# Kernel tuning notes

Hardware: AMD Instinct MI355X
Metric: run time of the kernel (lower is better)

Reference implementation:

```python
import jax, jax.numpy as jnp
import numpy as np

B, L, H, NH, NB = 16, 200, 128, 2, 2
ITEMS, SPAN = 50000, 256
NEG = -2.0**32 + 1.0  # mask value used by the torch module


def _ln(x, g, b, eps=1e-8):
    m = jnp.mean(x, axis=-1, keepdims=True)
    v = jnp.mean((x - m) ** 2, axis=-1, keepdims=True)
    return (x - m) / jnp.sqrt(v + eps) * g + b


def setup_inputs() -> dict:
    key = jax.random.key(0)
    ks = jax.random.split(key, 20)
    p = lambda k, s: (jax.random.normal(k, s, jnp.float32) * 0.02)
    item_emb = p(ks[0], (ITEMS + 1, H)).at[0].set(0.0)  # padding_idx=0
    return {
        "user_ids": jax.random.randint(ks[1], (B,), 0, 10000),
        "log_seqs": jax.random.randint(ks[2], (B, L), 0, ITEMS),
        "time_matrices": jax.random.randint(ks[3], (B, L, L), 0, SPAN),
        "pos_seqs": jax.random.randint(ks[4], (B, L), 0, ITEMS),
        "neg_seqs": jax.random.randint(ks[5], (B, L), 0, ITEMS),
        "item_emb": item_emb,
        "pos_K_emb": p(ks[6], (L, H)),
        "pos_V_emb": p(ks[7], (L, H)),
        "time_K_emb": p(ks[8], (SPAN + 1, H)),
        "time_V_emb": p(ks[9], (SPAN + 1, H)),
        "Wq": p(ks[10], (NB, H, H)), "bq": jnp.zeros((NB, H)),
        "Wk": p(ks[11], (NB, H, H)), "bk": jnp.zeros((NB, H)),
        "Wv": p(ks[12], (NB, H, H)), "bv": jnp.zeros((NB, H)),
        "ln1_g": jnp.ones((NB, H)), "ln1_b": jnp.zeros((NB, H)),
        "W1": p(ks[13], (NB, H, H)), "b1": jnp.zeros((NB, H)),
        "W2": p(ks[14], (NB, H, H)), "b2": jnp.zeros((NB, H)),
        "ln2_g": jnp.ones((NB, H)), "ln2_b": jnp.zeros((NB, H)),
        "lnf_g": jnp.ones((H,)), "lnf_b": jnp.zeros((H,)),
    }


def reference(user_ids, log_seqs, time_matrices, pos_seqs, neg_seqs,
              item_emb, pos_K_emb, pos_V_emb, time_K_emb, time_V_emb,
              Wq, bq, Wk, bk, Wv, bv, ln1_g, ln1_b,
              W1, b1, W2, b2, ln2_g, ln2_b, lnf_g, lnf_b):
    d = H // NH
    pad = (log_seqs == 0)                    # (B,L) timeline mask
    keep = (~pad)[..., None].astype(jnp.float32)

    seqs = item_emb[log_seqs] * jnp.sqrt(jnp.float32(H))
    seqs = seqs * keep
    posK = pos_K_emb.reshape(L, NH, d)       # same for every batch element
    posV = pos_V_emb.reshape(L, NH, d)
    tmK = time_K_emb[time_matrices].reshape(B, L, L, NH, d)  # (B,L,L,h,d)
    tmV = time_V_emb[time_matrices].reshape(B, L, L, NH, d)
    causal = ~jnp.tril(jnp.ones((L, L), dtype=bool))          # True = masked
    mask = pad[:, None, :, None] | causal[None, None, :, :]   # (B,1,L,L) row-mask | causal

    for i in range(NB):
        Q = (seqs @ Wq[i].T + bq[i]).reshape(B, L, NH, d)
        K = (seqs @ Wk[i].T + bk[i]).reshape(B, L, NH, d)
        V = (seqs @ Wv[i].T + bv[i]).reshape(B, L, NH, d)
        aw = jnp.einsum('bqhd,bkhd->bhqk', Q, K)
        aw = aw + jnp.einsum('bqhd,khd->bhqk', Q, posK)
        aw = aw + jnp.einsum('bqkhd,bqhd->bhqk', tmK, Q)
        aw = aw / jnp.sqrt(jnp.float32(d))
        aw = jnp.where(mask, NEG, aw)
        A = jax.nn.softmax(aw, axis=-1)                        # (B,h,L,L)
        out = jnp.einsum('bhqk,bkhd->bqhd', A, V)
        out = out + jnp.einsum('bhqk,khd->bqhd', A, posV)
        out = out + jnp.einsum('bhqk,bqkhd->bqhd', A, tmV)
        out = out.reshape(B, L, H)
        seqs = _ln(seqs + out, ln1_g[i], ln1_b[i])
        ffn = jax.nn.relu(seqs @ W1[i].T + b1[i]) @ W2[i].T + b2[i]
        seqs = _ln(seqs + ffn, ln2_g[i], ln2_b[i])
        seqs = seqs * keep

    log_feats = _ln(seqs, lnf_g, lnf_b)
    pos_logits = jnp.sum(log_feats * item_emb[pos_seqs], axis=-1)  # (B,L)
    neg_logits = jnp.sum(log_feats * item_emb[neg_seqs], axis=-1)
    return jnp.stack([pos_logits, neg_logits])  # (2,B,L)
```

## Files before the change

kernel.cpp:

```cpp
#include <hip/hip_runtime.h>
#include <hip/hip_bf16.h>
#include <math.h>

#define BB 16
#define LL 200
#define HH 128
#define DD 64
#define QT2 8
#define NQT2 25
#define NEGF -4294967295.0f
#define SQRTH 11.313708498984761f

__global__ __launch_bounds__(512) void k_qkv(float* __restrict__ seqs,
    const int* __restrict__ log_seqs, const float* __restrict__ item_emb, int do_embed,
    const float* __restrict__ Wq, const float* __restrict__ bq,
    const float* __restrict__ Wk, const float* __restrict__ bk,
    const float* __restrict__ Wv, const float* __restrict__ bv,
    const float* __restrict__ posK, const float* __restrict__ posV,
    float* __restrict__ Q, float* __restrict__ Kp, float* __restrict__ Vp) {
    __shared__ float s_lds[16][HH];
    int r0g = blockIdx.x * 16;
    int t = threadIdx.x;
    if (do_embed) {
        int r = t >> 5, d4 = t & 31;
        int id = log_seqs[r0g + r];
        float4 v = make_float4(0.f, 0.f, 0.f, 0.f);
        if (id != 0) {
            v = ((const float4*)(item_emb + id * HH))[d4];
            v.x *= SQRTH; v.y *= SQRTH; v.z *= SQRTH; v.w *= SQRTH;
        }
        *(float4*)&s_lds[r][d4 * 4] = v;
        ((float4*)(seqs + r0g * HH))[t] = v;
    } else {
        ((float4*)s_lds)[t] = ((const float4*)(seqs + r0g * HH))[t];
    }
    __syncthreads();
    int c = t & 127, rg = t >> 7;
    float aq[4] = {0.f, 0.f, 0.f, 0.f};
    float ak[4] = {0.f, 0.f, 0.f, 0.f};
    float av[4] = {0.f, 0.f, 0.f, 0.f};
    const float4* wq4 = (const float4*)(Wq + c * HH);
    const float4* wk4 = (const float4*)(Wk + c * HH);
    const float4* wv4 = (const float4*)(Wv + c * HH);
#pragma unroll 4
    for (int k4 = 0; k4 < HH / 4; ++k4) {
        float4 wq = wq4[k4], wk = wk4[k4], wv = wv4[k4];
#pragma unroll
        for (int r = 0; r < 4; ++r) {
            float4 s = *(const float4*)&s_lds[rg * 4 + r][k4 * 4];
            aq[r] += s.x * wq.x + s.y * wq.y + s.z * wq.z + s.w * wq.w;
            ak[r] += s.x * wk.x + s.y * wk.y + s.z * wk.z + s.w * wk.w;
            av[r] += s.x * wv.x + s.y * wv.y + s.z * wv.z + s.w * wv.w;
        }
    }
#pragma unroll
    for (int r = 0; r < 4; ++r) {
        int row = r0g + rg * 4 + r;
        int l = row % LL;
        Q[row * HH + c]  = aq[r] + bq[c];
        Kp[row * HH + c] = ak[r] + bk[c] + posK[l * HH + c];
        Vp[row * HH + c] = av[r] + bv[c] + posV[l * HH + c];
    }
}

__global__ __launch_bounds__(256) void k_proj(const float* __restrict__ Q,
    const float* __restrict__ timeK, float* __restrict__ projK) {
    int bh = blockIdx.x / 13, qt = blockIdx.x % 13;
    int b = bh >> 1, h = bh & 1;
    int qlo = qt * 16;
    __shared__ float Qs[16][68];
    __shared__ float TK[32][68];
    int t = threadIdx.x;
    {
        int r = t >> 4, d4 = t & 15;
        int q = qlo + r;
        float4 v = make_float4(0.f, 0.f, 0.f, 0.f);
        if (q < LL) v = ((const float4*)(Q + (b * LL + q) * HH + h * DD))[d4];
        *(float4*)&Qs[r][d4 * 4] = v;
    }
    int tq = t >> 4, ttl = t & 15;
    int q = qlo + tq;
    for (int c = 0; c < 9; ++c) {
        int base = c * 32;
        __syncthreads();
        for (int x = t; x < 512; x += 256) {
            int i = x >> 4, d4 = x & 15;
            int tt = base + i;
            if (tt < 257)
                *(float4*)&TK[i][d4 * 4] =
                    ((const float4*)(timeK + tt * HH + h * DD))[d4];
        }
        __syncthreads();
#pragma unroll
        for (int j = 0; j < 2; ++j) {
            int ti = ttl + 16 * j;
            int tt = base + ti;
            if (tt < 257 && q < LL) {
                float acc = 0.f;
#pragma unroll
                for (int d4 = 0; d4 < 16; ++d4) {
                    float4 qv = *(const float4*)&Qs[tq][d4 * 4];
                    float4 kv = *(const float4*)&TK[ti][d4 * 4];
                    acc += qv.x * kv.x + qv.y * kv.y + qv.z * kv.z + qv.w * kv.w;
                }
                projK[(bh * LL + q) * 257 + tt] = acc;
            }
        }
    }
}

__global__ __launch_bounds__(256) void k_attn(
    const float* __restrict__ Q, const float* __restrict__ Kp, const float* __restrict__ Vp,
    const float* __restrict__ projK, const float* __restrict__ timeV,
    const int* __restrict__ tm, const int* __restrict__ log_seqs,
    float* __restrict__ attnout) {
    int bh = blockIdx.x / NQT2, qt = blockIdx.x % NQT2;
    int b = bh >> 1, h = bh & 1;
    int qlo = qt * QT2;
    __shared__ float K_s[32][68];
    __shared__ float smemW[457 * 12];
    __shared__ float proj_T[257][9];
    __shared__ unsigned long long pm64[4];
    __shared__ int s_allmask;
#define WT(i, j) smemW[(i) * 12 + (j)]
    int t = threadIdx.x;
    int tq = t >> 5, lane = t & 31, g = tq;
    int q = qlo + tq;
    int qhi = qlo + QT2 - 1;

    {
        bool keep = (t < LL) && (log_seqs[b * LL + t] != 0);
        unsigned long long ball = __ballot(keep);
        if ((t & 63) == 0) pm64[t >> 6] = ball;
    }
    if (t == 0) s_allmask = 0;
    for (int x = t; x < 200 * 12; x += 256) smemW[x] = NEGF;
    for (int x = 200 * 12 + t; x < 457 * 12; x += 256) smemW[x] = 0.f;
    {
        const float* pbase = projK + (bh * LL + qlo) * 257;
        for (int x = t; x < 8 * 257; x += 256) {
            int qq = x / 257, tt = x - qq * 257;
            proj_T[tt][qq] = pbase[x];
        }
    }
    float4 qreg[16];
    {
        const float4* qp = (const float4*)(Q + (b * LL + q) * HH + h * DD);
#pragma unroll
        for (int d4 = 0; d4 < 16; ++d4) qreg[d4] = qp[d4];
    }
    const int* tmrow = tm + (b * LL + q) * LL;
    __syncthreads();

    int nkc = (qhi >> 5) + 1;
    for (int kc = 0; kc < nkc; ++kc) {
        int kbase = kc * 32;
        for (int x = t; x < 512; x += 256) {
            int i = x >> 4, d4 = x & 15;
            int k = kbase + i;
            if (k < LL)
                *(float4*)&K_s[i][d4 * 4] =
                    ((const float4*)(Kp + (b * LL + k) * HH + h * DD))[d4];
        }
        __syncthreads();
        int k = kbase + lane;
        if (k <= q && ((pm64[k >> 6] >> (k & 63)) & 1ull)) {
            float acc = 0.f;
#pragma unroll
            for (int d4 = 0; d4 < 16; ++d4) {
                float4 kv = *(const float4*)&K_s[lane][d4 * 4];
                acc += qreg[d4].x * kv.x + qreg[d4].y * kv.y +
                       qreg[d4].z * kv.z + qreg[d4].w * kv.w;
            }
            WT(k, tq) = (acc + proj_T[tmrow[k]][tq]) * 0.125f;
        }
        __syncthreads();
    }

    float mx = -INFINITY;
    for (int k = lane; k < LL; k += 32) mx = fmaxf(mx, WT(k, tq));
    mx = fmaxf(mx, __shfl_xor(mx, 1, 64));
    mx = fmaxf(mx, __shfl_xor(mx, 2, 64));
    mx = fmaxf(mx, __shfl_xor(mx, 4, 64));
    mx = fmaxf(mx, __shfl_xor(mx, 8, 64));
    mx = fmaxf(mx, __shfl_xor(mx, 16, 64));
    bool allmask = (mx == NEGF);
    float sum = 0.f;
    for (int k = lane; k < LL; k += 32) {
        float e = __expf(WT(k, tq) - mx);
        WT(k, tq) = e;
        sum += e;
    }
    sum += __shfl_xor(sum, 1, 64);
    sum += __shfl_xor(sum, 2, 64);
    sum += __shfl_xor(sum, 4, 64);
    sum += __shfl_xor(sum, 8, 64);
    sum += __shfl_xor(sum, 16, 64);
    float inv = 1.0f / sum;
    int klim = allmask ? LL : (q + 1);
    if (allmask && lane == 0) s_allmask = 1;
    for (int k = lane; k < LL; k += 32) {
        float p = WT(k, tq) * inv;
        WT(k, tq) = p;
        if (k < klim) atomicAdd(&WT(200 + tmrow[k], tq), p);
    }
    __syncthreads();

    int kmax = s_allmask ? LL : (qhi + 1);
    float a00=0.f,a01=0.f,a10=0.f,a11=0.f,a20=0.f,a21=0.f,a30=0.f,a31=0.f;
    float a40=0.f,a41=0.f,a50=0.f,a51=0.f,a60=0.f,a61=0.f,a70=0.f,a71=0.f;
#define PV_STEP(WROW, SRCPTR)                                            \
    {                                                                    \
        const float* wr = &WROW;                                         \
        float4 w0 = *(const float4*)wr;                                  \
        float4 w1 = *(const float4*)(wr + 4);                            \
        float2 vv = *(const float2*)(SRCPTR);                            \
        a00 += w0.x * vv.x; a01 += w0.x * vv.y;                          \
        a10 += w0.y * vv.x; a11 += w0.y * vv.y;                          \
        a20 += w0.z * vv.x; a21 += w0.z * vv.y;                          \
        a30 += w0.w * vv.x; a31 += w0.w * vv.y;                          \
        a40 += w1.x * vv.x; a41 += w1.x * vv.y;                          \
        a50 += w1.y * vv.x; a51 += w1.y * vv.y;                          \
        a60 += w1.z * vv.x; a61 += w1.z * vv.y;                          \
        a70 += w1.w * vv.x; a71 += w1.w * vv.y;                          \
    }
    for (int i = g; i < kmax; i += 8)
        PV_STEP(WT(i, 0), Vp + (b * LL + i) * HH + h * DD + lane * 2);
    for (int i = g; i < 257; i += 8)
        PV_STEP(WT(200 + i, 0), timeV + i * HH + h * DD + lane * 2);
#undef PV_STEP
    __syncthreads();
    float* part = smemW;
    part[g * 512 + 0 * 64 + lane * 2] = a00; part[g * 512 + 0 * 64 + lane * 2 + 1] = a01;
    part[g * 512 + 1 * 64 + lane * 2] = a10; part[g * 512 + 1 * 64 + lane * 2 + 1] = a11;
    part[g * 512 + 2 * 64 + lane * 2] = a20; part[g * 512 + 2 * 64 + lane * 2 + 1] = a21;
    part[g * 512 + 3 * 64 + lane * 2] = a30; part[g * 512 + 3 * 64 + lane * 2 + 1] = a31;
    part[g * 512 + 4 * 64 + lane * 2] = a40; part[g * 512 + 4 * 64 + lane * 2 + 1] = a41;
    part[g * 512 + 5 * 64 + lane * 2] = a50; part[g * 512 + 5 * 64 + lane * 2 + 1] = a51;
    part[g * 512 + 6 * 64 + lane * 2] = a60; part[g * 512 + 6 * 64 + lane * 2 + 1] = a61;
    part[g * 512 + 7 * 64 + lane * 2] = a70; part[g * 512 + 7 * 64 + lane * 2 + 1] = a71;
    __syncthreads();
    {
        float ox = 0.f, oy = 0.f;
#pragma unroll
        for (int gg = 0; gg < 8; ++gg) {
            ox += part[gg * 512 + tq * 64 + lane * 2];
            oy += part[gg * 512 + tq * 64 + lane * 2 + 1];
        }
        *(float2*)(attnout + (b * LL + q) * HH + h * DD + lane * 2) =
            make_float2(ox, oy);
    }
#undef WT
}

__global__ __launch_bounds__(256) void k_ffn_full(
    float* __restrict__ seqs, const float* __restrict__ AO,
    const float* __restrict__ g1, const float* __restrict__ be1,
    const float* __restrict__ W1, const float* __restrict__ b1,
    const float* __restrict__ W2, const float* __restrict__ b2,
    const float* __restrict__ g2, const float* __restrict__ be2,
    const int* __restrict__ log_seqs) {
    __shared__ float s_lds[8][HH];
    __shared__ float h_lds[8][HH];
    int r0g = blockIdx.x * 8;
    int t = threadIdx.x;
    {
        float4 a = ((const float4*)(seqs + r0g * HH))[t];
        float4 o = ((const float4*)(AO + r0g * HH))[t];
        a.x += o.x; a.y += o.y; a.z += o.z; a.w += o.w;
        ((float4*)s_lds)[t] = a;
    }
    __syncthreads();
    int w = t >> 6, lane = t & 63;
    int lrow = w * 2 + (lane >> 5), cl = lane & 31;
    {
        float sm = 0.f;
#pragma unroll
        for (int j = 0; j < 4; ++j) sm += s_lds[lrow][cl + 32 * j];
        sm += __shfl_xor(sm, 1, 64);
        sm += __shfl_xor(sm, 2, 64);
        sm += __shfl_xor(sm, 4, 64);
        sm += __shfl_xor(sm, 8, 64);
        sm += __shfl_xor(sm, 16, 64);
        float mean = sm * (1.0f / HH);
        float vr = 0.f;
#pragma unroll
        for (int j = 0; j < 4; ++j) {
            float d = s_lds[lrow][cl + 32 * j] - mean;
            vr += d * d;
        }
        vr += __shfl_xor(vr, 1, 64);
        vr += __shfl_xor(vr, 2, 64);
        vr += __shfl_xor(vr, 4, 64);
        vr += __shfl_xor(vr, 8, 64);
        vr += __shfl_xor(vr, 16, 64);
        float rstd = rsqrtf(vr * (1.0f / HH) + 1e-8f);
#pragma unroll
        for (int j = 0; j < 4; ++j) {
            int c = cl + 32 * j;
            s_lds[lrow][c] = (s_lds[lrow][c] - mean) * rstd * g1[c] + be1[c];
        }
    }
    __syncthreads();
    int c = t & 127, rg = t >> 7;
    float acc[4] = {0.f, 0.f, 0.f, 0.f};
    const float4* w14 = (const float4*)(W1 + c * HH);
#pragma unroll 4
    for (int k4 = 0; k4 < HH / 4; ++k4) {
        float4 ww = w14[k4];
#pragma unroll
        for (int r = 0; r < 4; ++r) {
            float4 s = *(const float4*)&s_lds[rg * 4 + r][k4 * 4];
            acc[r] += s.x * ww.x + s.y * ww.y + s.z * ww.z + s.w * ww.w;
        }
    }
#pragma unroll
    for (int r = 0; r < 4; ++r) h_lds[rg * 4 + r][c] = fmaxf(acc[r] + b1[c], 0.f);
    __syncthreads();
#pragma unroll
    for (int r = 0; r < 4; ++r) acc[r] = 0.f;
    const float4* w24 = (const float4*)(W2 + c * HH);
#pragma unroll 4
    for (int k4 = 0; k4 < HH / 4; ++k4) {
        float4 ww = w24[k4];
#pragma unroll
        for (int r = 0; r < 4; ++r) {
            float4 s = *(const float4*)&h_lds[rg * 4 + r][k4 * 4];
            acc[r] += s.x * ww.x + s.y * ww.y + s.z * ww.z + s.w * ww.w;
        }
    }
    __syncthreads();
#pragma unroll
    for (int r = 0; r < 4; ++r)
        h_lds[rg * 4 + r][c] = s_lds[rg * 4 + r][c] + acc[r] + b2[c];
    __syncthreads();
    {
        float sm = 0.f;
#pragma unroll
        for (int j = 0; j < 4; ++j) sm += h_lds[lrow][cl + 32 * j];
        sm += __shfl_xor(sm, 1, 64);
        sm += __shfl_xor(sm, 2, 64);
        sm += __shfl_xor(sm, 4, 64);
        sm += __shfl_xor(sm, 8, 64);
        sm += __shfl_xor(sm, 16, 64);
        float mean = sm * (1.0f / HH);
        float vr = 0.f;
#pragma unroll
        for (int j = 0; j < 4; ++j) {
            float d = h_lds[lrow][cl + 32 * j] - mean;
            vr += d * d;
        }
        vr += __shfl_xor(vr, 1, 64);
        vr += __shfl_xor(vr, 2, 64);
        vr += __shfl_xor(vr, 4, 64);
        vr += __shfl_xor(vr, 8, 64);
        vr += __shfl_xor(vr, 16, 64);
        float rstd = rsqrtf(vr * (1.0f / HH) + 1e-8f);
        float keep = (log_seqs[r0g + lrow] != 0) ? 1.0f : 0.0f;
#pragma unroll
        for (int j = 0; j < 4; ++j) {
            int cc = cl + 32 * j;
            float y = (h_lds[lrow][cc] - mean) * rstd * g2[cc] + be2[cc];
            seqs[(r0g + lrow) * HH + cc] = y * keep;
        }
    }
}

__global__ void k_final(const float* __restrict__ seqs,
                        const float* __restrict__ lnf_g, const float* __restrict__ lnf_b,
                        const float* __restrict__ item_emb,
                        const int* __restrict__ pos_seqs, const int* __restrict__ neg_seqs,
                        float* __restrict__ out) {
    __shared__ float red[2];
    int row = blockIdx.x;
    int t = threadIdx.x;
    float x = seqs[row * HH + t];
    float m = x;
    m += __shfl_xor(m, 1, 64); m += __shfl_xor(m, 2, 64); m += __shfl_xor(m, 4, 64);
    m += __shfl_xor(m, 8, 64); m += __shfl_xor(m, 16, 64); m += __shfl_xor(m, 32, 64);
    if ((t & 63) == 0) red[t >> 6] = m;
    __syncthreads();
    m = (red[0] + red[1]) * (1.0f / HH);
    float d = x - m;
    __syncthreads();
    float v2 = d * d;
    v2 += __shfl_xor(v2, 1, 64); v2 += __shfl_xor(v2, 2, 64); v2 += __shfl_xor(v2, 4, 64);
    v2 += __shfl_xor(v2, 8, 64); v2 += __shfl_xor(v2, 16, 64); v2 += __shfl_xor(v2, 32, 64);
    if ((t & 63) == 0) red[t >> 6] = v2;
    __syncthreads();
    float var = (red[0] + red[1]) * (1.0f / HH);
    float lf = d * rsqrtf(var + 1e-8f) * lnf_g[t] + lnf_b[t];
    int pid = pos_seqs[row];
    int nid = neg_seqs[row];
    float pp = lf * item_emb[pid * HH + t];
    float nn = lf * item_emb[nid * HH + t];
    __syncthreads();
    float ps = pp;
    ps += __shfl_xor(ps, 1, 64); ps += __shfl_xor(ps, 2, 64); ps += __shfl_xor(ps, 4, 64);
    ps += __shfl_xor(ps, 8, 64); ps += __shfl_xor(ps, 16, 64); ps += __shfl_xor(ps, 32, 64);
    if ((t & 63) == 0) red[t >> 6] = ps;
    __syncthreads();
    float ptot = red[0] + red[1];
    __syncthreads();
    float ns = nn;
    ns += __shfl_xor(ns, 1, 64); ns += __shfl_xor(ns, 2, 64); ns += __shfl_xor(ns, 4, 64);
    ns += __shfl_xor(ns, 8, 64); ns += __shfl_xor(ns, 16, 64); ns += __shfl_xor(ns, 32, 64);
    if ((t & 63) == 0) red[t >> 6] = ns;
    __syncthreads();
    float ntot = red[0] + red[1];
    if (t == 0) {
        out[row] = ptot;
        out[BB * LL + row] = ntot;
    }
}

extern "C" void kernel_launch(void* const* d_in, const int* in_sizes, int n_in,
                              void* d_out, int out_size, void* d_ws, size_t ws_size,
                              hipStream_t stream) {
    const int* log_seqs = (const int*)d_in[1];
    const int* tm       = (const int*)d_in[2];
    const int* pos_seqs = (const int*)d_in[3];
    const int* neg_seqs = (const int*)d_in[4];
    const float* item_emb = (const float*)d_in[5];
    const float* posK   = (const float*)d_in[6];
    const float* posV   = (const float*)d_in[7];
    const float* timeK  = (const float*)d_in[8];
    const float* timeV  = (const float*)d_in[9];
    const float* Wq = (const float*)d_in[10];
    const float* bq = (const float*)d_in[11];
    const float* Wk = (const float*)d_in[12];
    const float* bk = (const float*)d_in[13];
    const float* Wv = (const float*)d_in[14];
    const float* bv = (const float*)d_in[15];
    const float* ln1_g = (const float*)d_in[16];
    const float* ln1_b = (const float*)d_in[17];
    const float* W1 = (const float*)d_in[18];
    const float* b1 = (const float*)d_in[19];
    const float* W2 = (const float*)d_in[20];
    const float* b2 = (const float*)d_in[21];
    const float* ln2_g = (const float*)d_in[22];
    const float* ln2_b = (const float*)d_in[23];
    const float* lnf_g = (const float*)d_in[24];
    const float* lnf_b = (const float*)d_in[25];

    float* ws    = (float*)d_ws;
    float* seqs  = ws;
    float* Qb    = seqs + 409600;
    float* Kpb   = Qb + 409600;
    float* Vpb   = Kpb + 409600;
    float* AO    = Vpb + 409600;
    float* projK = AO + 409600;

    for (int i = 0; i < 2; ++i) {
        k_qkv<<<BB * LL / 16, 512, 0, stream>>>(seqs, log_seqs, item_emb, (i == 0) ? 1 : 0,
            Wq + i * HH * HH, bq + i * HH,
            Wk + i * HH * HH, bk + i * HH,
            Wv + i * HH * HH, bv + i * HH,
            posK, posV, Qb, Kpb, Vpb);
        k_proj<<<32 * 13, 256, 0, stream>>>(Qb, timeK, projK);
        k_attn<<<32 * NQT2, 256, 0, stream>>>(Qb, Kpb, Vpb, projK, timeV,
                                              tm, log_seqs, AO);
        k_ffn_full<<<BB * LL / 8, 256, 0, stream>>>(seqs, AO,
            ln1_g + i * HH, ln1_b + i * HH,
            W1 + i * HH * HH, b1 + i * HH,
            W2 + i * HH * HH, b2 + i * HH,
            ln2_g + i * HH, ln2_b + i * HH, log_seqs);
    }
    k_final<<<BB * LL, HH, 0, stream>>>(seqs, lnf_g, lnf_b, item_emb,
                                        pos_seqs, neg_seqs, (float*)d_out);
}
```

Baseline: 198.4 us.

## Fuse time-key projection into QKV kernel and final LN/logits into FFN kernel

```diff
diff --git a/kernel.cpp b/kernel.cpp
--- a/kernel.cpp
+++ b/kernel.cpp
@@ -11,14 +11,17 @@
 #define NEGF -4294967295.0f
 #define SQRTH 11.313708498984761f
 
-__global__ __launch_bounds__(512) void k_qkv(float* __restrict__ seqs,
+__global__ __launch_bounds__(512) void k_qkv_proj(float* __restrict__ seqs,
     const int* __restrict__ log_seqs, const float* __restrict__ item_emb, int do_embed,
     const float* __restrict__ Wq, const float* __restrict__ bq,
     const float* __restrict__ Wk, const float* __restrict__ bk,
     const float* __restrict__ Wv, const float* __restrict__ bv,
     const float* __restrict__ posK, const float* __restrict__ posV,
-    float* __restrict__ Q, float* __restrict__ Kp, float* __restrict__ Vp) {
+    const float* __restrict__ timeK,
+    float* __restrict__ Q, float* __restrict__ Kp, float* __restrict__ Vp,
+    float* __restrict__ projK) {
     __shared__ float s_lds[16][HH];
+    __shared__ float TK[32][132];
     int r0g = blockIdx.x * 16;
     int t = threadIdx.x;
     if (do_embed) {
@@ -53,57 +56,42 @@
             av[r] += s.x * wv.x + s.y * wv.y + s.z * wv.z + s.w * wv.w;
         }
     }
+    __syncthreads();
 #pragma unroll
     for (int r = 0; r < 4; ++r) {
         int row = r0g + rg * 4 + r;
         int l = row % LL;
-        Q[row * HH + c]  = aq[r] + bq[c];
+        float qv = aq[r] + bq[c];
+        Q[row * HH + c]  = qv;
+        s_lds[rg * 4 + r][c] = qv;
         Kp[row * HH + c] = ak[r] + bk[c] + posK[l * HH + c];
         Vp[row * HH + c] = av[r] + bv[c] + posV[l * HH + c];
     }
-}
-
-__global__ __launch_bounds__(256) void k_proj(const float* __restrict__ Q,
-    const float* __restrict__ timeK, float* __restrict__ projK) {
-    int bh = blockIdx.x / 13, qt = blockIdx.x % 13;
-    int b = bh >> 1, h = bh & 1;
-    int qlo = qt * 16;
-    __shared__ float Qs[16][68];
-    __shared__ float TK[32][68];
-    int t = threadIdx.x;
-    {
-        int r = t >> 4, d4 = t & 15;
-        int q = qlo + r;
-        float4 v = make_float4(0.f, 0.f, 0.f, 0.f);
-        if (q < LL) v = ((const float4*)(Q + (b * LL + q) * HH + h * DD))[d4];
-        *(float4*)&Qs[r][d4 * 4] = v;
-    }
-    int tq = t >> 4, ttl = t & 15;
-    int q = qlo + tq;
-    for (int c = 0; c < 9; ++c) {
-        int base = c * 32;
+    int tq = t >> 5, ttl = t & 31;
+    int row = r0g + tq;
+    int brow = row / LL, lrow = row - brow * LL;
+    for (int ch = 0; ch < 9; ++ch) {
+        int base = ch * 32;
         __syncthreads();
-        for (int x = t; x < 512; x += 256) {
-            int i = x >> 4, d4 = x & 15;
+        for (int x = t; x < 32 * 32; x += 512) {
+            int i = x >> 5, d4 = x & 31;
             int tt = base + i;
             if (tt < 257)
-                *(float4*)&TK[i][d4 * 4] =
-                    ((const float4*)(timeK + tt * HH + h * DD))[d4];
+                *(float4*)&TK[i][d4 * 4] = ((const float4*)(timeK + tt * HH))[d4];
         }
         __syncthreads();
-#pragma unroll
-        for (int j = 0; j < 2; ++j) {
-            int ti = ttl + 16 * j;
-            int tt = base + ti;
-            if (tt < 257 && q < LL) {
+        int tt = base + ttl;
+        if (tt < 257) {
+#pragma unroll
+            for (int h = 0; h < 2; ++h) {
                 float acc = 0.f;
 #pragma unroll
                 for (int d4 = 0; d4 < 16; ++d4) {
-                    float4 qv = *(const float4*)&Qs[tq][d4 * 4];
-                    float4 kv = *(const float4*)&TK[ti][d4 * 4];
+                    float4 qv = *(const float4*)&s_lds[tq][h * DD + d4 * 4];
+                    float4 kv = *(const float4*)&TK[ttl][h * DD + d4 * 4];
                     acc += qv.x * kv.x + qv.y * kv.y + qv.z * kv.z + qv.w * kv.w;
                 }
-                projK[(bh * LL + q) * 257 + tt] = acc;
+                projK[((brow * 2 + h) * LL + lrow) * 257 + tt] = acc;
             }
         }
     }
@@ -253,16 +241,20 @@
 #undef WT
 }
 
-__global__ __launch_bounds__(256) void k_ffn_full(
+__global__ __launch_bounds__(512) void k_ffn_full(
     float* __restrict__ seqs, const float* __restrict__ AO,
     const float* __restrict__ g1, const float* __restrict__ be1,
     const float* __restrict__ W1, const float* __restrict__ b1,
     const float* __restrict__ W2, const float* __restrict__ b2,
     const float* __restrict__ g2, const float* __restrict__ be2,
-    const int* __restrict__ log_seqs) {
-    __shared__ float s_lds[8][HH];
-    __shared__ float h_lds[8][HH];
-    int r0g = blockIdx.x * 8;
+    const int* __restrict__ log_seqs, int do_final,
+    const float* __restrict__ lnf_g, const float* __restrict__ lnf_b,
+    const float* __restrict__ item_emb,
+    const int* __restrict__ pos_seqs, const int* __restrict__ neg_seqs,
+    float* __restrict__ out) {
+    __shared__ float s_lds[16][HH];
+    __shared__ float h_lds[16][HH];
+    int r0g = blockIdx.x * 16;
     int t = threadIdx.x;
     {
         float4 a = ((const float4*)(seqs + r0g * HH))[t];
@@ -356,61 +348,63 @@
         vr += __shfl_xor(vr, 8, 64);
         vr += __shfl_xor(vr, 16, 64);
         float rstd = rsqrtf(vr * (1.0f / HH) + 1e-8f);
-        float keep = (log_seqs[r0g + lrow] != 0) ? 1.0f : 0.0f;
+        int row = r0g + lrow;
+        float keep = (log_seqs[row] != 0) ? 1.0f : 0.0f;
+        float y2[4];
 #pragma unroll
         for (int j = 0; j < 4; ++j) {
             int cc = cl + 32 * j;
-            float y = (h_lds[lrow][cc] - mean) * rstd * g2[cc] + be2[cc];
-            seqs[(r0g + lrow) * HH + cc] = y * keep;
-        }
-    }
-}
-
-__global__ void k_final(const float* __restrict__ seqs,
-                        const float* __restrict__ lnf_g, const float* __restrict__ lnf_b,
-                        const float* __restrict__ item_emb,
-                        const int* __restrict__ pos_seqs, const int* __restrict__ neg_seqs,
-                        float* __restrict__ out) {
-    __shared__ float red[2];
-    int row = blockIdx.x;
-    int t = threadIdx.x;
-    float x = seqs[row * HH + t];
-    float m = x;
-    m += __shfl_xor(m, 1, 64); m += __shfl_xor(m, 2, 64); m += __shfl_xor(m, 4, 64);
-    m += __shfl_xor(m, 8, 64); m += __shfl_xor(m, 16, 64); m += __shfl_xor(m, 32, 64);
-    if ((t & 63) == 0) red[t >> 6] = m;
-    __syncthreads();
-    m = (red[0] + red[1]) * (1.0f / HH);
-    float d = x - m;
-    __syncthreads();
-    float v2 = d * d;
-    v2 += __shfl_xor(v2, 1, 64); v2 += __shfl_xor(v2, 2, 64); v2 += __shfl_xor(v2, 4, 64);
-    v2 += __shfl_xor(v2, 8, 64); v2 += __shfl_xor(v2, 16, 64); v2 += __shfl_xor(v2, 32, 64);
-    if ((t & 63) == 0) red[t >> 6] = v2;
-    __syncthreads();
-    float var = (red[0] + red[1]) * (1.0f / HH);
-    float lf = d * rsqrtf(var + 1e-8f) * lnf_g[t] + lnf_b[t];
-    int pid = pos_seqs[row];
-    int nid = neg_seqs[row];
-    float pp = lf * item_emb[pid * HH + t];
-    float nn = lf * item_emb[nid * HH + t];
-    __syncthreads();
-    float ps = pp;
-    ps += __shfl_xor(ps, 1, 64); ps += __shfl_xor(ps, 2, 64); ps += __shfl_xor(ps, 4, 64);
-    ps += __shfl_xor(ps, 8, 64); ps += __shfl_xor(ps, 16, 64); ps += __shfl_xor(ps, 32, 64);
-    if ((t & 63) == 0) red[t >> 6] = ps;
-    __syncthreads();
-    float ptot = red[0] + red[1];
-    __syncthreads();
-    float ns = nn;
-    ns += __shfl_xor(ns, 1, 64); ns += __shfl_xor(ns, 2, 64); ns += __shfl_xor(ns, 4, 64);
-    ns += __shfl_xor(ns, 8, 64); ns += __shfl_xor(ns, 16, 64); ns += __shfl_xor(ns, 32, 64);
-    if ((t & 63) == 0) red[t >> 6] = ns;
-    __syncthreads();
-    float ntot = red[0] + red[1];
-    if (t == 0) {
-        out[row] = ptot;
-        out[BB * LL + row] = ntot;
+            y2[j] = ((h_lds[lrow][cc] - mean) * rstd * g2[cc] + be2[cc]) * keep;
+        }
+        if (!do_final) {
+#pragma unroll
+            for (int j = 0; j < 4; ++j)
+                seqs[row * HH + cl + 32 * j] = y2[j];
+        } else {
+            float sm2 = y2[0] + y2[1] + y2[2] + y2[3];
+            sm2 += __shfl_xor(sm2, 1, 64);
+            sm2 += __shfl_xor(sm2, 2, 64);
+            sm2 += __shfl_xor(sm2, 4, 64);
+            sm2 += __shfl_xor(sm2, 8, 64);
+            sm2 += __shfl_xor(sm2, 16, 64);
+            float mean2 = sm2 * (1.0f / HH);
+            float vr2 = 0.f;
+#pragma unroll
+            for (int j = 0; j < 4; ++j) {
+                float d = y2[j] - mean2;
+                vr2 += d * d;
+            }
+            vr2 += __shfl_xor(vr2, 1, 64);
+            vr2 += __shfl_xor(vr2, 2, 64);
+            vr2 += __shfl_xor(vr2, 4, 64);
+            vr2 += __shfl_xor(vr2, 8, 64);
+            vr2 += __shfl_xor(vr2, 16, 64);
+            float rstd2 = rsqrtf(vr2 * (1.0f / HH) + 1e-8f);
+            int pid = pos_seqs[row];
+            int nid = neg_seqs[row];
+            float pp = 0.f, nn = 0.f;
+#pragma unroll
+            for (int j = 0; j < 4; ++j) {
+                int cc = cl + 32 * j;
+                float lf = (y2[j] - mean2) * rstd2 * lnf_g[cc] + lnf_b[cc];
+                pp += lf * item_emb[pid * HH + cc];
+                nn += lf * item_emb[nid * HH + cc];
+            }
+            pp += __shfl_xor(pp, 1, 64);
+            pp += __shfl_xor(pp, 2, 64);
+            pp += __shfl_xor(pp, 4, 64);
+            pp += __shfl_xor(pp, 8, 64);
+            pp += __shfl_xor(pp, 16, 64);
+            nn += __shfl_xor(nn, 1, 64);
+            nn += __shfl_xor(nn, 2, 64);
+            nn += __shfl_xor(nn, 4, 64);
+            nn += __shfl_xor(nn, 8, 64);
+            nn += __shfl_xor(nn, 16, 64);
+            if (cl == 0) {
+                out[row] = pp;
+                out[BB * LL + row] = nn;
+            }
+        }
     }
 }
 
@@ -452,20 +446,20 @@
     float* projK = AO + 409600;
 
     for (int i = 0; i < 2; ++i) {
-        k_qkv<<<BB * LL / 16, 512, 0, stream>>>(seqs, log_seqs, item_emb, (i == 0) ? 1 : 0,
+        k_qkv_proj<<<BB * LL / 16, 512, 0, stream>>>(seqs, log_seqs, item_emb,
+            (i == 0) ? 1 : 0,
             Wq + i * HH * HH, bq + i * HH,
             Wk + i * HH * HH, bk + i * HH,
             Wv + i * HH * HH, bv + i * HH,
-            posK, posV, Qb, Kpb, Vpb);
-        k_proj<<<32 * 13, 256, 0, stream>>>(Qb, timeK, projK);
+            posK, posV, timeK, Qb, Kpb, Vpb, projK);
         k_attn<<<32 * NQT2, 256, 0, stream>>>(Qb, Kpb, Vpb, projK, timeV,
                                               tm, log_seqs, AO);
-        k_ffn_full<<<BB * LL / 8, 256, 0, stream>>>(seqs, AO,
+        k_ffn_full<<<BB * LL / 16, 512, 0, stream>>>(seqs, AO,
             ln1_g + i * HH, ln1_b + i * HH,
             W1 + i * HH * HH, b1 + i * HH,
             W2 + i * HH * HH, b2 + i * HH,
-            ln2_g + i * HH, ln2_b + i * HH, log_seqs);
-    }
-    k_final<<<BB * LL, HH, 0, stream>>>(seqs, lnf_g, lnf_b, item_emb,
-                                        pos_seqs, neg_seqs, (float*)d_out);
+            ln2_g + i * HH, ln2_b + i * HH, log_seqs,
+            (i == 1) ? 1 : 0, lnf_g, lnf_b, item_emb,
+            pos_seqs, neg_seqs, (float*)d_out);
+    }
 }
```

Measured after the change: 191.4 us. -3.5%, faster.
